# Kernel tuning notes

Hardware: AMD Instinct MI355X
Metric: run time of the kernel (lower is better)

Reference implementation:

```python
import jax, jax.numpy as jnp
import numpy as np

NI = 2048           # per-node feature dim
H = 2 * NI          # flattened per-sample GRU state (2 nodes)
BS = 4096
NO = 1
NUM_ROUNDS = 2


def setup_inputs() -> dict:
    key = jax.random.key(0)
    ks = jax.random.split(key, 8)
    s_ih = 1.0 / np.sqrt(H)
    features = jax.random.normal(ks[0], (BS, 2, NI), dtype=jnp.float32)
    # torch.nn.GRUCell(H, H): weight_ih [3H, H], weight_hh [3H, H], biases [3H]
    W_ih = jax.random.uniform(ks[1], (3 * H, H), minval=-s_ih, maxval=s_ih, dtype=jnp.float32)
    b_ih = jax.random.uniform(ks[2], (3 * H,), minval=-s_ih, maxval=s_ih, dtype=jnp.float32)
    W_hh = jax.random.uniform(ks[3], (3 * H, H), minval=-s_ih, maxval=s_ih, dtype=jnp.float32)
    b_hh = jax.random.uniform(ks[4], (3 * H,), minval=-s_ih, maxval=s_ih, dtype=jnp.float32)
    # fc = nn.Linear(2*ni, no)
    fc_w = jax.random.uniform(ks[5], (NO, H), minval=-s_ih, maxval=s_ih, dtype=jnp.float32)
    fc_b = jax.random.uniform(ks[6], (NO,), minval=-s_ih, maxval=s_ih, dtype=jnp.float32)
    return {"features": features, "W_ih": W_ih, "b_ih": b_ih,
            "W_hh": W_hh, "b_hh": b_hh, "fc_w": fc_w, "fc_b": fc_b}


def _gru_cell(x, h, W_ih, b_ih, W_hh, b_hh):
    # torch GRUCell semantics
    gi = x @ W_ih.T + b_ih              # [bs, 3H]
    gh = h @ W_hh.T + b_hh              # [bs, 3H]
    i_r, i_z, i_n = jnp.split(gi, 3, axis=-1)
    h_r, h_z, h_n = jnp.split(gh, 3, axis=-1)
    r = jax.nn.sigmoid(i_r + h_r)
    z = jax.nn.sigmoid(i_z + h_z)
    n = jnp.tanh(i_n + r * h_n)
    return (1.0 - z) * n + z * h


def reference(features, W_ih, b_ih, W_hh, b_hh, fc_w, fc_b):
    bs = features.shape[0]
    ni = features.shape[2]
    h = features.reshape(bs, -1)        # [bs, 2*ni] = node0 || node1
    for _ in range(NUM_ROUNDS):
        # fully-connected 2-node graph, sum-aggregate of neighbor messages:
        # node0 receives h1, node1 receives h0 -> x is the half-swap of h
        x = jnp.concatenate([h[:, ni:], h[:, :ni]], axis=-1)
        h = _gru_cell(x, h, W_ih, b_ih, W_hh, b_hh)
    return h @ fc_w.T + fc_b            # [bs, no]
```

## Files before the change

### kernel.cpp

```cpp
#include <hip/hip_runtime.h>


typedef __bf16 bf16x8 __attribute__((ext_vector_type(8)));
typedef float  f32x4  __attribute__((ext_vector_type(4)));
typedef unsigned short u16x4 __attribute__((ext_vector_type(4)));

#define HH    4096
#define NI_D  2048
#define N3H   12288
#define N6H   24576
#define BSZ   4096
#define BM    256
#define BN    256
#define BK    64
#define MT    (BSZ / BM)
#define NT    (N6H / BN)
#define GRID_GEMM (MT * NT)
#define NKT   (HH / BK)

__device__ __forceinline__ unsigned short f2bf(float f) {
  unsigned u = __float_as_uint(f);
  u += 0x7FFFu + ((u >> 16) & 1u);
  return (unsigned short)(u >> 16);
}
__device__ __forceinline__ float bf2f(unsigned short s) {
  return __uint_as_float(((unsigned)s) << 16);
}

__device__ __forceinline__ void gload16(const void* g, void* l) {
  void* gv = (void*)g;
  __builtin_amdgcn_global_load_lds(
      (__attribute__((address_space(1))) unsigned int*)gv,
      (__attribute__((address_space(3))) unsigned int*)l,
      16, 0, 0);
}

__global__ void __launch_bounds__(256)
convert_weights(const float* __restrict__ Wih, const float* __restrict__ Whh,
                unsigned short* __restrict__ Wc)
{
  int idx = (blockIdx.x * 256 + threadIdx.x) << 2;
  int j = idx >> 12;
  int k = idx & 4095;
  const float* src;
  if (j < N3H) src = Wih + (size_t)j * HH + ((k + NI_D) & (HH - 1));
  else         src = Whh + (size_t)(j - N3H) * HH + k;
  f32x4 v = *(const f32x4*)src;
  u16x4 o = { f2bf(v[0]), f2bf(v[1]), f2bf(v[2]), f2bf(v[3]) };
  *(u16x4*)(Wc + idx) = o;
}

__global__ void __launch_bounds__(256)
cast_f32_bf16(const float* __restrict__ src, unsigned short* __restrict__ dst)
{
  int i = (blockIdx.x * 256 + threadIdx.x) << 2;
  f32x4 v = *(const f32x4*)(src + i);
  u16x4 o = { f2bf(v[0]), f2bf(v[1]), f2bf(v[2]), f2bf(v[3]) };
  *(u16x4*)(dst + i) = o;
}

__device__ __forceinline__ void stageA(const char* a_base, char* lds, int ldst,
                                       int d, int kt, int g) {
  int kc = (kt < NKT) ? kt : 0;
  gload16(a_base + (size_t)kc * 128 + (size_t)g * 524288,
          lds + d * 32768 + g * 8192 + ldst);
}
__device__ __forceinline__ void stageB(const char* b_base, char* lds, int ldst,
                                       int d, int kt, int g) {
  int kc = (kt < NKT) ? kt : 0;
  gload16(b_base + (size_t)kc * 128 + (size_t)g * 524288,
          lds + 65536 + d * 32768 + g * 8192 + ldst);
}

template <int MB>
__device__ __forceinline__ void mfma16(f32x4 (&acc)[8][4],
                                       const bf16x8 (&aA)[2], const bf16x8 (&aB)[2],
                                       const bf16x8 (&bfr)[4][2]) {
  __builtin_amdgcn_s_setprio(1);
#pragma unroll
  for (int ks = 0; ks < 2; ++ks)
#pragma unroll
    for (int nf = 0; nf < 4; ++nf) {
      acc[MB][nf]     = __builtin_amdgcn_mfma_f32_16x16x32_bf16(
                          aA[ks], bfr[nf][ks], acc[MB][nf], 0, 0, 0);
      acc[MB + 1][nf] = __builtin_amdgcn_mfma_f32_16x16x32_bf16(
                          aB[ks], bfr[nf][ks], acc[MB + 1][nf], 0, 0, 0);
    }
  __builtin_amdgcn_s_setprio(0);
}

#define BAR   __builtin_amdgcn_s_barrier()
#define LGKM0 do { asm volatile("s_waitcnt lgkmcnt(0)" ::: "memory");          \
                   __builtin_amdgcn_sched_barrier(0); } while (0)

template <int D>
__device__ __forceinline__ void kblock(char* lds, const char* a_base,
                                       const char* b_base, int ldst,
                                       int aro, int bro, int offk0, int offk1,
                                       int t1, int t2, f32x4 (&acc)[8][4]) {
  const char* LA = lds + D * 32768 + aro;
  const char* LB = lds + 65536 + D * 32768 + bro;
  bf16x8 bfr[4][2];

  {
#pragma unroll
    for (int nf = 0; nf < 4; ++nf) {
      bfr[nf][0] = *(const bf16x8*)(LB + nf * 2048 + offk0);
      bfr[nf][1] = *(const bf16x8*)(LB + nf * 2048 + offk1);
    }
    bf16x8 aA[2], aB[2];
    aA[0] = *(const bf16x8*)(LA + 6 * 2048 + offk0);
    aA[1] = *(const bf16x8*)(LA + 6 * 2048 + offk1);
    aB[0] = *(const bf16x8*)(LA + 7 * 2048 + offk0);
    aB[1] = *(const bf16x8*)(LA + 7 * 2048 + offk1);
    stageA(a_base, lds, ldst, D ^ 1, t1, 0);
    stageA(a_base, lds, ldst, D ^ 1, t1, 2);
    asm volatile("s_waitcnt lgkmcnt(8)" ::: "memory");
    BAR; LGKM0;
    mfma16<6>(acc, aA, aB, bfr);
    BAR;
  }
  {
    bf16x8 aA[2], aB[2];
    aA[0] = *(const bf16x8*)(LA + 4 * 2048 + offk0);
    aA[1] = *(const bf16x8*)(LA + 4 * 2048 + offk1);
    aB[0] = *(const bf16x8*)(LA + 5 * 2048 + offk0);
    aB[1] = *(const bf16x8*)(LA + 5 * 2048 + offk1);
    stageB(b_base, lds, ldst, D, t2, 0);
    stageB(b_base, lds, ldst, D, t2, 1);
    BAR; LGKM0;
    mfma16<4>(acc, aA, aB, bfr);
    BAR;
  }
  {
    bf16x8 aA[2], aB[2];
    aA[0] = *(const bf16x8*)(LA + 2 * 2048 + offk0);
    aA[1] = *(const bf16x8*)(LA + 2 * 2048 + offk1);
    aB[0] = *(const bf16x8*)(LA + 3 * 2048 + offk0);
    aB[1] = *(const bf16x8*)(LA + 3 * 2048 + offk1);
    stageB(b_base, lds, ldst, D, t2, 2);
    stageB(b_base, lds, ldst, D, t2, 3);
    BAR; LGKM0;
    mfma16<2>(acc, aA, aB, bfr);
    BAR;
  }
  {
    bf16x8 aA[2], aB[2];
    aA[0] = *(const bf16x8*)(LA + 0 * 2048 + offk0);
    aA[1] = *(const bf16x8*)(LA + 0 * 2048 + offk1);
    aB[0] = *(const bf16x8*)(LA + 1 * 2048 + offk0);
    aB[1] = *(const bf16x8*)(LA + 1 * 2048 + offk1);
    stageA(a_base, lds, ldst, D, t2, 1);
    stageA(a_base, lds, ldst, D, t2, 3);
    BAR; LGKM0;
    mfma16<0>(acc, aA, aB, bfr);
    asm volatile("s_waitcnt vmcnt(6)" ::: "memory");
    BAR;
  }
}

__global__ void __launch_bounds__(512, 2)
gemm_bt(const unsigned short* __restrict__ A,
        const unsigned short* __restrict__ B,
        unsigned short* __restrict__ C)
{
  __shared__ alignas(16) char lds[131072];

  int bid = blockIdx.x;
  int wg  = (bid & 7) * (GRID_GEMM / 8) + (bid >> 3);
  int nt  = wg / MT;
  int mt  = wg % MT;
  int m0  = mt * BM;
  int n0  = nt * BN;

  int t  = threadIdx.x;
  int wv = t >> 6;
  int l  = t & 63;
  int wm = wv >> 2;
  int wn = wv & 3;

  int rloc   = wv * 8 + (l >> 3);
  int sg_col = ((l & 7) ^ (l >> 3)) << 4;
  const char* a_base = (const char*)A + (size_t)(m0 + rloc) * 8192 + sg_col;
  const char* b_base = (const char*)B + (size_t)(n0 + rloc) * 8192 + sg_col;
  int ldst = wv * 1024;

  int offk0 = (((l >> 4) << 4)) ^ ((l & 7) << 4);
  int offk1 = offk0 ^ 64;
  int aro = (wm * 128 + (l & 15)) * 128;
  int bro = (wn * 64  + (l & 15)) * 128;

  f32x4 acc[8][4] = {};

#pragma unroll
  for (int g = 0; g < 4; ++g) stageA(a_base, lds, ldst, 0, 0, g);
#pragma unroll
  for (int g = 0; g < 4; ++g) stageB(b_base, lds, ldst, 0, 0, g);
#pragma unroll
  for (int g = 0; g < 4; ++g) stageB(b_base, lds, ldst, 1, 1, g);
  stageA(a_base, lds, ldst, 1, 1, 1);
  stageA(a_base, lds, ldst, 1, 1, 3);
  asm volatile("s_waitcnt vmcnt(6)" ::: "memory");
  BAR;

#pragma unroll 1
  for (int tt = 0; tt < NKT; tt += 2) {
    kblock<0>(lds, a_base, b_base, ldst, aro, bro, offk0, offk1,
              tt + 1, tt + 2, acc);
    kblock<1>(lds, a_base, b_base, ldst, aro, bro, offk0, offk1,
              tt + 2, tt + 3, acc);
  }
  asm volatile("s_waitcnt vmcnt(0)" ::: "memory");

  int crow = m0 + wm * 128 + ((l >> 4) << 2);
  int ccol = n0 + wn * 64 + (l & 15);
#pragma unroll
  for (int mf = 0; mf < 8; ++mf)
#pragma unroll
    for (int nf = 0; nf < 4; ++nf)
#pragma unroll
      for (int i = 0; i < 4; ++i)
        C[(size_t)(crow + mf * 16 + i) * N6H + (ccol + nf * 16)] =
            f2bf(acc[mf][nf][i]);
}

__global__ void __launch_bounds__(256)
gru_update(const unsigned short* __restrict__ C, const float* __restrict__ h_old,
           const float* __restrict__ b_ih, const float* __restrict__ b_hh,
           float* __restrict__ h_new, unsigned short* __restrict__ h_bf)
{
  int idx = blockIdx.x * 256 + threadIdx.x;
  int b = idx >> 10;
  int j = (idx & 1023) << 2;
  const unsigned short* Cr = C + (size_t)b * N6H;
  u16x4 gir = *(const u16x4*)(Cr + j);
  u16x4 giz = *(const u16x4*)(Cr + HH + j);
  u16x4 gin = *(const u16x4*)(Cr + 2 * HH + j);
  u16x4 ghr = *(const u16x4*)(Cr + 3 * HH + j);
  u16x4 ghz = *(const u16x4*)(Cr + 4 * HH + j);
  u16x4 ghn = *(const u16x4*)(Cr + 5 * HH + j);
  f32x4 bir = *(const f32x4*)(b_ih + j);
  f32x4 biz = *(const f32x4*)(b_ih + HH + j);
  f32x4 bin = *(const f32x4*)(b_ih + 2 * HH + j);
  f32x4 bhr = *(const f32x4*)(b_hh + j);
  f32x4 bhz = *(const f32x4*)(b_hh + HH + j);
  f32x4 bhn = *(const f32x4*)(b_hh + 2 * HH + j);
  f32x4 ho  = *(const f32x4*)(h_old + (size_t)b * HH + j);
  f32x4 hv; u16x4 hb;
#pragma unroll
  for (int e = 0; e < 4; ++e) {
    float r = 1.f / (1.f + expf(-(bf2f(gir[e]) + bir[e] + bf2f(ghr[e]) + bhr[e])));
    float z = 1.f / (1.f + expf(-(bf2f(giz[e]) + biz[e] + bf2f(ghz[e]) + bhz[e])));
    float n = tanhf(bf2f(gin[e]) + bin[e] + r * (bf2f(ghn[e]) + bhn[e]));
    float h = (1.f - z) * n + z * ho[e];
    hv[e] = h; hb[e] = f2bf(h);
  }
  *(f32x4*)(h_new + (size_t)b * HH + j) = hv;
  *(u16x4*)(h_bf + (size_t)b * HH + j)  = hb;
}

__global__ void __launch_bounds__(256)
final_fc(const float* __restrict__ h, const float* __restrict__ fcw,
         const float* __restrict__ fcb, float* __restrict__ out)
{
  int b = blockIdx.x, t = threadIdx.x;
  const float* row = h + (size_t)b * HH;
  float s = 0.f;
#pragma unroll
  for (int i = 0; i < 4; ++i) {
    int v4 = t + i * 256;
    f32x4 hv = *(const f32x4*)(row + v4 * 4);
    f32x4 wv = *(const f32x4*)(fcw + v4 * 4);
    s += hv[0] * wv[0] + hv[1] * wv[1] + hv[2] * wv[2] + hv[3] * wv[3];
  }
#pragma unroll
  for (int off = 32; off > 0; off >>= 1) s += __shfl_down(s, off);
  __shared__ float red[4];
  if ((t & 63) == 0) red[t >> 6] = s;
  __syncthreads();
  if (t == 0) out[b] = red[0] + red[1] + red[2] + red[3] + fcb[0];
}

extern "C" void kernel_launch(void* const* d_in, const int* in_sizes, int n_in,
                              void* d_out, int out_size, void* d_ws, size_t ws_size,
                              hipStream_t stream)
{
  const float* feat = (const float*)d_in[0];
  const float* Wih  = (const float*)d_in[1];
  const float* bih  = (const float*)d_in[2];
  const float* Whh  = (const float*)d_in[3];
  const float* bhh  = (const float*)d_in[4];
  const float* fcw  = (const float*)d_in[5];
  const float* fcb  = (const float*)d_in[6];
  float* out = (float*)d_out;

  char* ws = (char*)d_ws;
  unsigned short* Wc   = (unsigned short*)ws;
  unsigned short* Cbuf = (unsigned short*)(ws + 201326592);
  unsigned short* hb   = (unsigned short*)(ws + 402653184);
  float*          hf   = (float*)(ws + 436207616);

  convert_weights<<<98304, 256, 0, stream>>>(Wih, Whh, Wc);
  cast_f32_bf16<<<16384, 256, 0, stream>>>(feat, hb);

  gemm_bt<<<GRID_GEMM, 512, 0, stream>>>(hb, Wc, Cbuf);
  gru_update<<<16384, 256, 0, stream>>>(Cbuf, feat, bih, bhh, hf, hb);

  gemm_bt<<<GRID_GEMM, 512, 0, stream>>>(hb, Wc, Cbuf);
  gru_update<<<16384, 256, 0, stream>>>(Cbuf, hf, bih, bhh, hf, hb);

  final_fc<<<4096, 256, 0, stream>>>(hf, fcw, fcb, out);
}
```

Before: 1.570 ms.

## Fuse prep casts, fuse final GRU step with FC, reorder GEMM fragment schedule

Merges the weight and feature bf16 casts into a single prep launch. The second GRU update is fused with the final FC reduction, reduced with atomics into a zeroed output, so the fp32 hidden-state buffer is never written. The GEMM inner k-block is restructured into quadrant MFMA groups with different LDS fragment reuse and staging order. The fused path reads the previous hidden state in bf16, which costs precision, and atomics make the summation order nondeterministic.

After: 1.546 ms. Within noise of the previous version (-1.5%).

```diff
diff --git a/kernel.cpp b/kernel.cpp
--- a/kernel.cpp
+++ b/kernel.cpp
@@ -18,6 +18,9 @@
 #define GRID_GEMM (MT * NT)
 #define NKT   (HH / BK)
 
+#define NB_W  98304
+#define NB_C  16384
+
 __device__ __forceinline__ unsigned short f2bf(float f) {
   unsigned u = __float_as_uint(f);
   u += 0x7FFFu + ((u >> 16) & 1u);
@@ -36,27 +39,27 @@
 }
 
 __global__ void __launch_bounds__(256)
-convert_weights(const float* __restrict__ Wih, const float* __restrict__ Whh,
-                unsigned short* __restrict__ Wc)
-{
-  int idx = (blockIdx.x * 256 + threadIdx.x) << 2;
-  int j = idx >> 12;
-  int k = idx & 4095;
-  const float* src;
-  if (j < N3H) src = Wih + (size_t)j * HH + ((k + NI_D) & (HH - 1));
-  else         src = Whh + (size_t)(j - N3H) * HH + k;
-  f32x4 v = *(const f32x4*)src;
-  u16x4 o = { f2bf(v[0]), f2bf(v[1]), f2bf(v[2]), f2bf(v[3]) };
-  *(u16x4*)(Wc + idx) = o;
-}
-
-__global__ void __launch_bounds__(256)
-cast_f32_bf16(const float* __restrict__ src, unsigned short* __restrict__ dst)
-{
-  int i = (blockIdx.x * 256 + threadIdx.x) << 2;
-  f32x4 v = *(const f32x4*)(src + i);
-  u16x4 o = { f2bf(v[0]), f2bf(v[1]), f2bf(v[2]), f2bf(v[3]) };
-  *(u16x4*)(dst + i) = o;
+prep(const float* __restrict__ Wih, const float* __restrict__ Whh,
+     const float* __restrict__ feat,
+     unsigned short* __restrict__ Wc, unsigned short* __restrict__ hb)
+{
+  int bid = blockIdx.x;
+  if (bid < NB_W) {
+    int idx = (bid * 256 + threadIdx.x) << 2;
+    int j = idx >> 12;
+    int k = idx & 4095;
+    const float* src;
+    if (j < N3H) src = Wih + (size_t)j * HH + ((k + NI_D) & (HH - 1));
+    else         src = Whh + (size_t)(j - N3H) * HH + k;
+    f32x4 v = *(const f32x4*)src;
+    u16x4 o = { f2bf(v[0]), f2bf(v[1]), f2bf(v[2]), f2bf(v[3]) };
+    *(u16x4*)(Wc + idx) = o;
+  } else {
+    int i = ((bid - NB_W) * 256 + threadIdx.x) << 2;
+    f32x4 v = *(const f32x4*)(feat + i);
+    u16x4 o = { f2bf(v[0]), f2bf(v[1]), f2bf(v[2]), f2bf(v[3]) };
+    *(u16x4*)(hb + i) = o;
+  }
 }
 
 __device__ __forceinline__ void stageA(const char* a_base, char* lds, int ldst,
@@ -72,20 +75,19 @@
           lds + 65536 + d * 32768 + g * 8192 + ldst);
 }
 
-template <int MB>
-__device__ __forceinline__ void mfma16(f32x4 (&acc)[8][4],
-                                       const bf16x8 (&aA)[2], const bf16x8 (&aB)[2],
-                                       const bf16x8 (&bfr)[4][2]) {
+template <int MB, int NB>
+__device__ __forceinline__ void mfmaQ(f32x4 (&acc)[8][4],
+                                      const bf16x8 (&af)[4][2],
+                                      const bf16x8 (&bf)[2][2]) {
   __builtin_amdgcn_s_setprio(1);
 #pragma unroll
   for (int ks = 0; ks < 2; ++ks)
 #pragma unroll
-    for (int nf = 0; nf < 4; ++nf) {
-      acc[MB][nf]     = __builtin_amdgcn_mfma_f32_16x16x32_bf16(
-                          aA[ks], bfr[nf][ks], acc[MB][nf], 0, 0, 0);
-      acc[MB + 1][nf] = __builtin_amdgcn_mfma_f32_16x16x32_bf16(
-                          aB[ks], bfr[nf][ks], acc[MB + 1][nf], 0, 0, 0);
-    }
+    for (int mf = 0; mf < 4; ++mf)
+#pragma unroll
+      for (int nf = 0; nf < 2; ++nf)
+        acc[MB + mf][NB + nf] = __builtin_amdgcn_mfma_f32_16x16x32_bf16(
+            af[mf][ks], bf[nf][ks], acc[MB + mf][NB + nf], 0, 0, 0);
   __builtin_amdgcn_s_setprio(0);
 }
 
@@ -100,63 +102,53 @@
                                        int t1, int t2, f32x4 (&acc)[8][4]) {
   const char* LA = lds + D * 32768 + aro;
   const char* LB = lds + 65536 + D * 32768 + bro;
-  bf16x8 bfr[4][2];
-
-  {
-#pragma unroll
-    for (int nf = 0; nf < 4; ++nf) {
-      bfr[nf][0] = *(const bf16x8*)(LB + nf * 2048 + offk0);
-      bfr[nf][1] = *(const bf16x8*)(LB + nf * 2048 + offk1);
-    }
-    bf16x8 aA[2], aB[2];
-    aA[0] = *(const bf16x8*)(LA + 6 * 2048 + offk0);
-    aA[1] = *(const bf16x8*)(LA + 6 * 2048 + offk1);
-    aB[0] = *(const bf16x8*)(LA + 7 * 2048 + offk0);
-    aB[1] = *(const bf16x8*)(LA + 7 * 2048 + offk1);
-    stageA(a_base, lds, ldst, D ^ 1, t1, 0);
-    stageA(a_base, lds, ldst, D ^ 1, t1, 2);
-    asm volatile("s_waitcnt lgkmcnt(8)" ::: "memory");
-    BAR; LGKM0;
-    mfma16<6>(acc, aA, aB, bfr);
-    BAR;
-  }
-  {
-    bf16x8 aA[2], aB[2];
-    aA[0] = *(const bf16x8*)(LA + 4 * 2048 + offk0);
-    aA[1] = *(const bf16x8*)(LA + 4 * 2048 + offk1);
-    aB[0] = *(const bf16x8*)(LA + 5 * 2048 + offk0);
-    aB[1] = *(const bf16x8*)(LA + 5 * 2048 + offk1);
-    stageB(b_base, lds, ldst, D, t2, 0);
-    stageB(b_base, lds, ldst, D, t2, 1);
-    BAR; LGKM0;
-    mfma16<4>(acc, aA, aB, bfr);
-    BAR;
-  }
-  {
-    bf16x8 aA[2], aB[2];
-    aA[0] = *(const bf16x8*)(LA + 2 * 2048 + offk0);
-    aA[1] = *(const bf16x8*)(LA + 2 * 2048 + offk1);
-    aB[0] = *(const bf16x8*)(LA + 3 * 2048 + offk0);
-    aB[1] = *(const bf16x8*)(LA + 3 * 2048 + offk1);
-    stageB(b_base, lds, ldst, D, t2, 2);
-    stageB(b_base, lds, ldst, D, t2, 3);
-    BAR; LGKM0;
-    mfma16<2>(acc, aA, aB, bfr);
-    BAR;
-  }
-  {
-    bf16x8 aA[2], aB[2];
-    aA[0] = *(const bf16x8*)(LA + 0 * 2048 + offk0);
-    aA[1] = *(const bf16x8*)(LA + 0 * 2048 + offk1);
-    aB[0] = *(const bf16x8*)(LA + 1 * 2048 + offk0);
-    aB[1] = *(const bf16x8*)(LA + 1 * 2048 + offk1);
-    stageA(a_base, lds, ldst, D, t2, 1);
-    stageA(a_base, lds, ldst, D, t2, 3);
-    BAR; LGKM0;
-    mfma16<0>(acc, aA, aB, bfr);
-    asm volatile("s_waitcnt vmcnt(6)" ::: "memory");
-    BAR;
-  }
+  bf16x8 a47[4][2], a03[4][2], b01[2][2], b23[2][2];
+
+#pragma unroll
+  for (int mf = 0; mf < 4; ++mf) {
+    a47[mf][0] = *(const bf16x8*)(LA + (4 + mf) * 2048 + offk0);
+    a47[mf][1] = *(const bf16x8*)(LA + (4 + mf) * 2048 + offk1);
+  }
+#pragma unroll
+  for (int nf = 0; nf < 2; ++nf) {
+    b01[nf][0] = *(const bf16x8*)(LB + nf * 2048 + offk0);
+    b01[nf][1] = *(const bf16x8*)(LB + nf * 2048 + offk1);
+  }
+  stageA(a_base, lds, ldst, D ^ 1, t1, 0);
+  stageA(a_base, lds, ldst, D ^ 1, t1, 2);
+  asm volatile("s_waitcnt lgkmcnt(8)" ::: "memory");
+  BAR; LGKM0;
+  mfmaQ<4, 0>(acc, a47, b01);
+  BAR;
+
+#pragma unroll
+  for (int nf = 0; nf < 2; ++nf) {
+    b23[nf][0] = *(const bf16x8*)(LB + (2 + nf) * 2048 + offk0);
+    b23[nf][1] = *(const bf16x8*)(LB + (2 + nf) * 2048 + offk1);
+  }
+  stageA(a_base, lds, ldst, D, t2, 1);
+  stageA(a_base, lds, ldst, D, t2, 3);
+  BAR; LGKM0;
+  mfmaQ<4, 2>(acc, a47, b23);
+  BAR;
+
+#pragma unroll
+  for (int mf = 0; mf < 4; ++mf) {
+    a03[mf][0] = *(const bf16x8*)(LA + mf * 2048 + offk0);
+    a03[mf][1] = *(const bf16x8*)(LA + mf * 2048 + offk1);
+  }
+  stageB(b_base, lds, ldst, D, t2, 0);
+  stageB(b_base, lds, ldst, D, t2, 1);
+  BAR; LGKM0;
+  mfmaQ<0, 0>(acc, a03, b01);
+  BAR;
+
+  stageB(b_base, lds, ldst, D, t2, 2);
+  stageB(b_base, lds, ldst, D, t2, 3);
+  BAR;
+  mfmaQ<0, 2>(acc, a03, b23);
+  asm volatile("s_waitcnt vmcnt(6)" ::: "memory");
+  BAR;
 }
 
 __global__ void __launch_bounds__(512, 2)
@@ -185,7 +177,7 @@
   const char* b_base = (const char*)B + (size_t)(n0 + rloc) * 8192 + sg_col;
   int ldst = wv * 1024;
 
-  int offk0 = (((l >> 4) << 4)) ^ ((l & 7) << 4);
+  int offk0 = ((l >> 4) << 4) ^ ((l & 7) << 4);
   int offk1 = offk0 ^ 64;
   int aro = (wm * 128 + (l & 15)) * 128;
   int bro = (wn * 64  + (l & 15)) * 128;
@@ -196,10 +188,10 @@
   for (int g = 0; g < 4; ++g) stageA(a_base, lds, ldst, 0, 0, g);
 #pragma unroll
   for (int g = 0; g < 4; ++g) stageB(b_base, lds, ldst, 0, 0, g);
-#pragma unroll
-  for (int g = 0; g < 4; ++g) stageB(b_base, lds, ldst, 1, 1, g);
   stageA(a_base, lds, ldst, 1, 1, 1);
   stageA(a_base, lds, ldst, 1, 1, 3);
+#pragma unroll
+  for (int g = 0; g < 4; ++g) stageB(b_base, lds, ldst, 1, 1, g);
   asm volatile("s_waitcnt vmcnt(6)" ::: "memory");
   BAR;
 
@@ -225,9 +217,9 @@
 }
 
 __global__ void __launch_bounds__(256)
-gru_update(const unsigned short* __restrict__ C, const float* __restrict__ h_old,
-           const float* __restrict__ b_ih, const float* __restrict__ b_hh,
-           float* __restrict__ h_new, unsigned short* __restrict__ h_bf)
+gru1(const unsigned short* __restrict__ C, const float* __restrict__ h_old,
+     const float* __restrict__ b_ih, const float* __restrict__ b_hh,
+     unsigned short* __restrict__ h_bf)
 {
   int idx = blockIdx.x * 256 + threadIdx.x;
   int b = idx >> 10;
@@ -246,39 +238,61 @@
   f32x4 bhz = *(const f32x4*)(b_hh + HH + j);
   f32x4 bhn = *(const f32x4*)(b_hh + 2 * HH + j);
   f32x4 ho  = *(const f32x4*)(h_old + (size_t)b * HH + j);
-  f32x4 hv; u16x4 hb;
+  u16x4 hb;
 #pragma unroll
   for (int e = 0; e < 4; ++e) {
     float r = 1.f / (1.f + expf(-(bf2f(gir[e]) + bir[e] + bf2f(ghr[e]) + bhr[e])));
     float z = 1.f / (1.f + expf(-(bf2f(giz[e]) + biz[e] + bf2f(ghz[e]) + bhz[e])));
     float n = tanhf(bf2f(gin[e]) + bin[e] + r * (bf2f(ghn[e]) + bhn[e]));
-    float h = (1.f - z) * n + z * ho[e];
-    hv[e] = h; hb[e] = f2bf(h);
-  }
-  *(f32x4*)(h_new + (size_t)b * HH + j) = hv;
-  *(u16x4*)(h_bf + (size_t)b * HH + j)  = hb;
+    hb[e] = f2bf((1.f - z) * n + z * ho[e]);
+  }
+  *(u16x4*)(h_bf + (size_t)b * HH + j) = hb;
 }
 
 __global__ void __launch_bounds__(256)
-final_fc(const float* __restrict__ h, const float* __restrict__ fcw,
-         const float* __restrict__ fcb, float* __restrict__ out)
-{
-  int b = blockIdx.x, t = threadIdx.x;
-  const float* row = h + (size_t)b * HH;
+gru2_fc(const unsigned short* __restrict__ C,
+        const unsigned short* __restrict__ h_old_bf,
+        const float* __restrict__ b_ih, const float* __restrict__ b_hh,
+        const float* __restrict__ fcw, const float* __restrict__ fcb,
+        float* __restrict__ out)
+{
+  int idx = blockIdx.x * 256 + threadIdx.x;
+  int b = idx >> 10;
+  int j = (idx & 1023) << 2;
+  const unsigned short* Cr = C + (size_t)b * N6H;
+  u16x4 gir = *(const u16x4*)(Cr + j);
+  u16x4 giz = *(const u16x4*)(Cr + HH + j);
+  u16x4 gin = *(const u16x4*)(Cr + 2 * HH + j);
+  u16x4 ghr = *(const u16x4*)(Cr + 3 * HH + j);
+  u16x4 ghz = *(const u16x4*)(Cr + 4 * HH + j);
+  u16x4 ghn = *(const u16x4*)(Cr + 5 * HH + j);
+  f32x4 bir = *(const f32x4*)(b_ih + j);
+  f32x4 biz = *(const f32x4*)(b_ih + HH + j);
+  f32x4 bin = *(const f32x4*)(b_ih + 2 * HH + j);
+  f32x4 bhr = *(const f32x4*)(b_hh + j);
+  f32x4 bhz = *(const f32x4*)(b_hh + HH + j);
+  f32x4 bhn = *(const f32x4*)(b_hh + 2 * HH + j);
+  u16x4 hob = *(const u16x4*)(h_old_bf + (size_t)b * HH + j);
+  f32x4 fw  = *(const f32x4*)(fcw + j);
   float s = 0.f;
 #pragma unroll
-  for (int i = 0; i < 4; ++i) {
-    int v4 = t + i * 256;
-    f32x4 hv = *(const f32x4*)(row + v4 * 4);
-    f32x4 wv = *(const f32x4*)(fcw + v4 * 4);
-    s += hv[0] * wv[0] + hv[1] * wv[1] + hv[2] * wv[2] + hv[3] * wv[3];
+  for (int e = 0; e < 4; ++e) {
+    float r = 1.f / (1.f + expf(-(bf2f(gir[e]) + bir[e] + bf2f(ghr[e]) + bhr[e])));
+    float z = 1.f / (1.f + expf(-(bf2f(giz[e]) + biz[e] + bf2f(ghz[e]) + bhz[e])));
+    float n = tanhf(bf2f(gin[e]) + bin[e] + r * (bf2f(ghn[e]) + bhn[e]));
+    float h = (1.f - z) * n + z * bf2f(hob[e]);
+    s += h * fw[e];
   }
 #pragma unroll
   for (int off = 32; off > 0; off >>= 1) s += __shfl_down(s, off);
   __shared__ float red[4];
-  if ((t & 63) == 0) red[t >> 6] = s;
+  if ((threadIdx.x & 63) == 0) red[threadIdx.x >> 6] = s;
   __syncthreads();
-  if (t == 0) out[b] = red[0] + red[1] + red[2] + red[3] + fcb[0];
+  if (threadIdx.x == 0) {
+    float v = red[0] + red[1] + red[2] + red[3];
+    if ((blockIdx.x & 3) == 0) v += fcb[0];
+    atomicAdd(&out[b], v);
+  }
 }
 
 extern "C" void kernel_launch(void* const* d_in, const int* in_sizes, int n_in,
@@ -298,16 +312,13 @@
   unsigned short* Wc   = (unsigned short*)ws;
   unsigned short* Cbuf = (unsigned short*)(ws + 201326592);
   unsigned short* hb   = (unsigned short*)(ws + 402653184);
-  float*          hf   = (float*)(ws + 436207616);
-
-  convert_weights<<<98304, 256, 0, stream>>>(Wih, Whh, Wc);
-  cast_f32_bf16<<<16384, 256, 0, stream>>>(feat, hb);
+
+  hipMemsetAsync(out, 0, (size_t)out_size * sizeof(float), stream);
+  prep<<<NB_W + NB_C, 256, 0, stream>>>(Wih, Whh, feat, Wc, hb);
 
   gemm_bt<<<GRID_GEMM, 512, 0, stream>>>(hb, Wc, Cbuf);
-  gru_update<<<16384, 256, 0, stream>>>(Cbuf, feat, bih, bhh, hf, hb);
+  gru1<<<16384, 256, 0, stream>>>(Cbuf, feat, bih, bhh, hb);
 
   gemm_bt<<<GRID_GEMM, 512, 0, stream>>>(hb, Wc, Cbuf);
-  gru_update<<<16384, 256, 0, stream>>>(Cbuf, hf, bih, bhh, hf, hb);
-
-  final_fc<<<4096, 256, 0, stream>>>(hf, fcw, fcb, out);
-}
+  gru2_fc<<<16384, 256, 0, stream>>>(Cbuf, hb, bih, bhh, fcw, fcb, out);
+}
```
